# Kernel tuning notes

Measured on AMD Instinct MI355X. Metric: run time of the kernel, lower is better.

Reference implementation:

```python
import jax, jax.numpy as jnp
import numpy as np

D_MODEL = 1024
NUM_HEADS = 16
D_K = D_MODEL // NUM_HEADS


def setup_inputs() -> dict:
    key = jax.random.key(0)
    ks = jax.random.split(key, 8)
    B, S, D = 4, 2048, D_MODEL
    scale = 1.0 / np.sqrt(D)
    return {
        "query": jax.random.normal(ks[0], (B, S, D), dtype=jnp.float32),
        "key": jax.random.normal(ks[1], (B, S, D), dtype=jnp.float32),
        "value": jax.random.normal(ks[2], (B, S, D), dtype=jnp.float32),
        "Wq": jax.random.normal(ks[3], (D, D), dtype=jnp.float32) * scale,
        "bq": jnp.zeros((D,), dtype=jnp.float32),
        "Wk": jax.random.normal(ks[4], (D, D), dtype=jnp.float32) * scale,
        "bk": jnp.zeros((D,), dtype=jnp.float32),
        "Wv": jax.random.normal(ks[5], (D, D), dtype=jnp.float32) * scale,
        "bv": jnp.zeros((D,), dtype=jnp.float32),
        "Wo": jax.random.normal(ks[6], (D, D), dtype=jnp.float32) * scale,
        "bo": jnp.zeros((D,), dtype=jnp.float32),
    }


def reference(query, key, value, Wq, bq, Wk, bk, Wv, bv, Wo, bo):
    B, S, D = query.shape
    H, dk = NUM_HEADS, D_K

    def proj(x, W, b):
        # nn.Linear: x @ W.T + b, then split heads -> [B, H, S, dk]
        y = jnp.einsum("bsd,ed->bse", x, W) + b
        return y.reshape(B, -1, H, dk).transpose(0, 2, 1, 3)

    Q = proj(query, Wq, bq)
    K = proj(key, Wk, bk)
    V = proj(value, Wv, bv)

    scores = jnp.einsum("bhqd,bhkd->bhqk", Q, K) / np.sqrt(dk).astype(jnp.float32)
    attn = jax.nn.softmax(scores, axis=-1)
    out = jnp.einsum("bhqk,bhkd->bhqd", attn, V)  # [B, H, S, dk]
    out = out.transpose(0, 2, 1, 3).reshape(B, -1, D)
    return jnp.einsum("bsd,ed->bse", out, Wo) + bo
```

## Files before the change

### kernel.cpp

```cpp
#include <hip/hip_runtime.h>
#include <hip/hip_bf16.h>

typedef unsigned short u16;
typedef __attribute__((ext_vector_type(8))) short bf16x8;
typedef __attribute__((ext_vector_type(4))) short bf16x4;
typedef __attribute__((ext_vector_type(4))) float f32x4;

#define LOG2E_OVER8 0.18033688011112043f

__device__ __forceinline__ float ex2(float x) {
#if __has_builtin(__builtin_amdgcn_exp2f)
    return __builtin_amdgcn_exp2f(x);
#else
    float r;
    asm volatile("v_exp_f32 %0, %1" : "=v"(r) : "v"(x));
    return r;
#endif
}

__device__ __forceinline__ u16 f2bf(float f) {
    unsigned u = __float_as_uint(f);
    u += 0x7FFFu + ((u >> 16) & 1u);
    return (u16)(u >> 16);
}

__device__ __forceinline__ unsigned pk_rtz(float lo, float hi) {
    return __builtin_amdgcn_perm(__float_as_uint(hi), __float_as_uint(lo), 0x07060302u);
}
__device__ __forceinline__ bf16x8 pack8(float a0, float a1, float a2, float a3,
                                        float a4, float a5, float a6, float a7) {
    unsigned p[4];
    p[0] = pk_rtz(a0, a1);
    p[1] = pk_rtz(a2, a3);
    p[2] = pk_rtz(a4, a5);
    p[3] = pk_rtz(a6, a7);
    bf16x8 r;
    __builtin_memcpy(&r, p, 16);
    return r;
}

__device__ __forceinline__ unsigned pk_rhu(float lo, float hi) {
    unsigned a = __float_as_uint(lo) + 0x8000u;
    unsigned b = __float_as_uint(hi) + 0x8000u;
    return __builtin_amdgcn_perm(b, a, 0x07060302u);
}

__device__ __forceinline__ f32x4 mfma32(bf16x8 a, bf16x8 b, f32x4 c) {
    return __builtin_amdgcn_mfma_f32_16x16x32_bf16(a, b, c, 0, 0, 0);
}

__device__ __forceinline__ void gload16(const void* g, void* l) {
    __builtin_amdgcn_global_load_lds((const __attribute__((address_space(1))) unsigned int*)g,
                                     (__attribute__((address_space(3))) unsigned int*)l,
                                     16, 0, 0);
}

__global__ __launch_bounds__(256) void cvt_w4(const float* __restrict__ a, const float* __restrict__ b,
                                              const float* __restrict__ c, const float* __restrict__ d,
                                              u16* __restrict__ out) {
    const float* src = (blockIdx.y == 0) ? a : (blockIdx.y == 1) ? b : (blockIdx.y == 2) ? c : d;
    size_t i = ((size_t)blockIdx.x * 256 + threadIdx.x) * 4;
    float4 v = *(const float4*)(src + i);
    bf16x4 o;
    o[0] = (short)f2bf(v.x); o[1] = (short)f2bf(v.y);
    o[2] = (short)f2bf(v.z); o[3] = (short)f2bf(v.w);
    *(bf16x4*)(out + (size_t)blockIdx.y * (1024ull * 1024) + i) = o;
}

struct GemmAcc { f32x4 a[4][4]; };

__device__ __forceinline__ void gemm_core(const u16* __restrict__ A, const u16* __restrict__ Bt,
                                          u16* As, u16* Bs, int bm, int bn, GemmAcc& acc) {
    constexpr int K = 1024;
    const int tid = threadIdx.x;
    const int lane = tid & 63;
    const int lr = lane & 15, lg = lane >> 4;
    const int l7 = lr & 7;

    for (int i = 0; i < 4; i++)
        for (int j = 0; j < 4; j++) acc.a[i][j] = (f32x4){0.f, 0.f, 0.f, 0.f};

    const int row0 = tid >> 3, u0 = tid & 7;
    const int su = (u0 ^ (row0 & 7)) * 8;
    size_t a_off[4], b_off[4];
#pragma unroll
    for (int i = 0; i < 4; i++) {
        a_off[i] = (size_t)(bm + i * 32 + row0) * K + su;
        b_off[i] = (size_t)(bn + i * 32 + row0) * K + su;
    }
    const int c0 = tid * 8;
    const int wid = tid >> 6, wr = wid >> 1, wc = wid & 1;

    for (int kt = 0; kt < K; kt += 64) {
#pragma unroll
        for (int i = 0; i < 4; i++) gload16(A + a_off[i] + kt, &As[i * 2048 + c0]);
#pragma unroll
        for (int i = 0; i < 4; i++) gload16(Bt + b_off[i] + kt, &Bs[i * 2048 + c0]);
        __syncthreads();
#pragma unroll
        for (int kh = 0; kh < 2; kh++) {
            const int fu = ((kh * 4 + lg) ^ l7) * 8;
            bf16x8 aF[4], bF[4];
#pragma unroll
            for (int mi = 0; mi < 4; mi++) aF[mi] = *(const bf16x8*)&As[(wr * 64 + mi * 16 + lr) * 64 + fu];
#pragma unroll
            for (int ni = 0; ni < 4; ni++) bF[ni] = *(const bf16x8*)&Bs[(wc * 64 + ni * 16 + lr) * 64 + fu];
#pragma unroll
            for (int mi = 0; mi < 4; mi++)
#pragma unroll
                for (int ni = 0; ni < 4; ni++) acc.a[mi][ni] = mfma32(aF[mi], bF[ni], acc.a[mi][ni]);
        }
        __syncthreads();
    }
}

template<int MODE>
__global__ __launch_bounds__(256, 2) void gemm_f32a(const float* __restrict__ A, const u16* __restrict__ Bt,
                                                    const float* __restrict__ bias, u16* __restrict__ Cout,
                                                    float scale) {
    __shared__ u16 As[128 * 64];
    __shared__ u16 Bs[128 * 64];
    const int tid = threadIdx.x;
    const int bid = blockIdx.x;
    const int m_ = bid & 63, n_ = bid >> 6;
    const int bm = m_ * 128, bn = n_ * 128;
    const int lane = tid & 63;
    const int lr = lane & 15, lg = lane >> 4;
    const int l7 = lr & 7;

    f32x4 acc[4][4];
    for (int i = 0; i < 4; i++)
        for (int j = 0; j < 4; j++) acc[i][j] = (f32x4){0.f, 0.f, 0.f, 0.f};

    const int row0 = tid >> 3, u0 = tid & 7;
    const int su = (u0 ^ (row0 & 7)) * 8;
    size_t b_off[4];
#pragma unroll
    for (int i = 0; i < 4; i++) b_off[i] = (size_t)(bn + i * 32 + row0) * 1024 + su;
    const int c0 = tid * 8;

    const int ar = tid >> 4;
    const size_t a_base = (size_t)(bm + ar) * 1024 + (tid & 15) * 4;
    const int wds = ar * 64 + ((((tid & 15) >> 1) ^ (ar & 7)) << 3) + (tid & 1) * 4;

    float4 fA[2][8];
#pragma unroll
    for (int j = 0; j < 8; ++j) fA[0][j] = *(const float4*)(A + a_base + (size_t)j * 16384);

    const int wid = tid >> 6, wr = wid >> 1, wc = wid & 1;

#pragma unroll 2
    for (int t = 0; t < 16; ++t) {
        const int cur = t & 1;
        const int kt = t * 64;
#pragma unroll
        for (int i = 0; i < 4; i++) gload16(Bt + b_off[i] + kt, &Bs[i * 2048 + c0]);
        const int ktn = ((t + 1) & 15) * 64;
#pragma unroll
        for (int j = 0; j < 8; ++j) fA[cur ^ 1][j] = *(const float4*)(A + a_base + ktn + (size_t)j * 16384);
#pragma unroll
        for (int j = 0; j < 8; ++j) {
            const float4 v = fA[cur][j];
            unsigned p2[2];
            p2[0] = pk_rhu(v.x, v.y);
            p2[1] = pk_rhu(v.z, v.w);
            __builtin_memcpy(&As[wds + j * 1024], p2, 8);
        }
        __syncthreads();
#pragma unroll
        for (int kh = 0; kh < 2; kh++) {
            const int fu = ((kh * 4 + lg) ^ l7) * 8;
            bf16x8 aF[4], bF[4];
#pragma unroll
            for (int mi = 0; mi < 4; mi++) aF[mi] = *(const bf16x8*)&As[(wr * 64 + mi * 16 + lr) * 64 + fu];
#pragma unroll
            for (int ni = 0; ni < 4; ni++) bF[ni] = *(const bf16x8*)&Bs[(wc * 64 + ni * 16 + lr) * 64 + fu];
#pragma unroll
            for (int mi = 0; mi < 4; mi++)
#pragma unroll
                for (int ni = 0; ni < 4; ni++) acc[mi][ni] = mfma32(aF[mi], bF[ni], acc[mi][ni]);
        }
        __syncthreads();
    }

#pragma unroll
    for (int ni = 0; ni < 4; ni++) {
        const int n = bn + wc * 64 + ni * 16 + lr;
        const float bv = bias[n];
#pragma unroll
        for (int mi = 0; mi < 4; mi++) {
            const int mbase = bm + wr * 64 + mi * 16 + lg * 4;
#pragma unroll
            for (int r = 0; r < 4; r++) {
                const int m = mbase + r;
                const float v = acc[mi][ni][r] + bv;
                if (MODE == 1) {
                    Cout[(size_t)m * 1024 + n] = f2bf(v * scale);
                } else {
                    const int bq_ = m >> 11, kk = m & 2047, kb = kk >> 6, k64 = kk & 63;
                    const int hh = n >> 6, dd = n & 63;
                    const int ks = k64 >> 4, g = (k64 >> 2) & 3, rr = k64 & 3;
                    const int unit = ((ks >> 1) << 2) | g;
                    const int jj = ((ks & 1) << 2) | rr;
                    Cout[((size_t)((bq_ * 16 + hh) * 32 + kb)) * 4096 +
                         dd * 64 + ((unit ^ (dd & 7)) << 3) + jj] = f2bf(v);
                }
            }
        }
    }
}

__global__ __launch_bounds__(256) void gemm_out(const u16* __restrict__ A, const u16* __restrict__ Bt,
                                                const float* __restrict__ bias, float* __restrict__ Cout) {
    __shared__ u16 As[128 * 64];
    __shared__ u16 Bs[128 * 64];
    const int bid = blockIdx.x;
    const int m_ = bid & 63, n_ = bid >> 6;
    const int bm = m_ * 128, bn = n_ * 128;
    GemmAcc acc;
    gemm_core(A, Bt, As, Bs, bm, bn, acc);

    const int lane = threadIdx.x & 63, wid = threadIdx.x >> 6;
    const int wr = wid >> 1, wc = wid & 1;
    const int lr = lane & 15, lg = lane >> 4;
#pragma unroll
    for (int ni = 0; ni < 4; ni++) {
        const int n = bn + wc * 64 + ni * 16 + lr;
        const float bv = bias[n];
#pragma unroll
        for (int mi = 0; mi < 4; mi++) {
            const int mbase = bm + wr * 64 + mi * 16 + lg * 4;
#pragma unroll
            for (int r = 0; r < 4; r++)
                Cout[(size_t)(mbase + r) * 1024 + n] = acc.a[mi][ni][r] + bv;
        }
    }
}

__global__ __launch_bounds__(256, 2) void attn_fwd(const u16* __restrict__ Qp, const u16* __restrict__ Kp,
                                                   const u16* __restrict__ VTb, u16* __restrict__ AO) {
    __shared__ u16 kt[2][4096];
    __shared__ u16 vt[2][4096];
    const int tid = threadIdx.x;
    const int lane = tid & 63, wave = tid >> 6;
    const int lr = lane & 15, lg = lane >> 4;
    const int l7 = lr & 7;
    const int bh = blockIdx.x & 63, b = bh >> 4, h = bh & 15;
    const int q0 = (blockIdx.x >> 6) * 256 + wave * 64;

    const u16* qbase = Qp + (size_t)(b * 2048 + q0) * 1024 + h * 64;
    bf16x8 qf[4][2];
#pragma unroll
    for (int qt = 0; qt < 4; qt++)
#pragma unroll
        for (int hf = 0; hf < 2; hf++)
            qf[qt][hf] = *(const bf16x8*)(qbase + (size_t)(qt * 16 + lr) * 1024 + hf * 32 + lg * 8);

    const int srow = tid >> 3;
    const int scol = (((tid & 7) ^ (srow & 7)) * 8);
    const u16* kg = Kp + (size_t)(b * 2048 + srow) * 1024 + h * 64 + scol;
    const u16* vg = VTb + (size_t)(b * 16 + h) * 32 * 4096 + tid * 8;
    const int ldst = tid * 8;

#define STAGE(buf, kb_)                                                       \
    do {                                                                      \
        gload16(kg + (size_t)(kb_) * 64 * 1024,        &kt[buf][ldst]);       \
        gload16(kg + (size_t)((kb_) * 64 + 32) * 1024, &kt[buf][2048 + ldst]);\
        gload16(vg + (size_t)(kb_) * 4096,             &vt[buf][ldst]);       \
        gload16(vg + (size_t)(kb_) * 4096 + 2048,      &vt[buf][2048 + ldst]);\
    } while (0)

    f32x4 lsacc[4];
    f32x4 ot[4][4];
#pragma unroll
    for (int qt = 0; qt < 4; qt++) {
        lsacc[qt] = (f32x4){0.f, 0.f, 0.f, 0.f};
#pragma unroll
        for (int dt = 0; dt < 4; dt++) ot[qt][dt] = (f32x4){0.f, 0.f, 0.f, 0.f};
    }

    bf16x8 ones8;
#pragma unroll
    for (int i = 0; i < 8; i++) ones8[i] = (short)0x3F80;

    STAGE(0, 0);
    __syncthreads();
    int cur = 0;

    const f32x4 zero = (f32x4){0.f, 0.f, 0.f, 0.f};
    const int ku0 = (lg ^ l7) * 8;
    const int ku1 = ((4 + lg) ^ l7) * 8;

#pragma unroll 2
    for (int it = 0; it < 32; ++it) {
        if (it < 31) STAGE(cur ^ 1, it + 1);

        const u16* kl = &kt[cur][0];
        const u16* vl = &vt[cur][0];

        f32x4 s[4][4];
        __builtin_amdgcn_s_setprio(1);
#pragma unroll
        for (int ks = 0; ks < 4; ++ks) {
            const int rbase = (ks * 16 + lr) * 64;
            bf16x8 kf0 = *(const bf16x8*)&kl[rbase + ku0];
            bf16x8 kf1 = *(const bf16x8*)&kl[rbase + ku1];
#pragma unroll
            for (int qt = 0; qt < 4; ++qt) {
                s[qt][ks] = mfma32(kf0, qf[qt][0], zero);
                s[qt][ks] = mfma32(kf1, qf[qt][1], s[qt][ks]);
            }
        }
        __builtin_amdgcn_s_setprio(0);

        bf16x8 pf[4][2];
#pragma unroll
        for (int qt = 0; qt < 4; ++qt) {
#pragma unroll
            for (int kh = 0; kh < 2; ++kh) {
                const f32x4 sa = s[qt][2 * kh], sb = s[qt][2 * kh + 1];
                pf[qt][kh] = pack8(ex2(sa[0]), ex2(sa[1]), ex2(sa[2]), ex2(sa[3]),
                                   ex2(sb[0]), ex2(sb[1]), ex2(sb[2]), ex2(sb[3]));
                lsacc[qt] = mfma32(ones8, pf[qt][kh], lsacc[qt]);
            }
        }

        __builtin_amdgcn_s_setprio(1);
#pragma unroll
        for (int dt = 0; dt < 4; ++dt) {
            const int vrow = (dt * 16 + lr) * 64;
            bf16x8 vf0 = *(const bf16x8*)&vl[vrow + ku0];
            bf16x8 vf1 = *(const bf16x8*)&vl[vrow + ku1];
#pragma unroll
            for (int qt = 0; qt < 4; ++qt) {
                ot[qt][dt] = mfma32(vf0, pf[qt][0], ot[qt][dt]);
                ot[qt][dt] = mfma32(vf1, pf[qt][1], ot[qt][dt]);
            }
        }
        __builtin_amdgcn_s_setprio(0);

        __syncthreads();
        cur ^= 1;
    }

    float inv[4];
#pragma unroll
    for (int qt = 0; qt < 4; qt++) inv[qt] = 1.0f / lsacc[qt][0];
    u16* t_ = &kt[0][0] + wave * 2048;
#pragma unroll
    for (int pass = 0; pass < 2; ++pass) {
        __syncthreads();
#pragma unroll
        for (int qh = 0; qh < 2; ++qh) {
            const int qt = pass * 2 + qh;
#pragma unroll
            for (int dt = 0; dt < 4; ++dt)
#pragma unroll
                for (int r = 0; r < 4; ++r)
                    t_[(qh * 16 + lr) * 64 + dt * 16 + lg * 4 + r] = f2bf(ot[qt][dt][r] * inv[qt]);
        }
        __syncthreads();
        const int qq = lane >> 1, dseg = (lane & 1) * 32;
        u16* dst = AO + (size_t)(b * 2048 + q0 + pass * 32 + qq) * 1024 + h * 64 + dseg;
        bf16x8 o_[4];
#pragma unroll
        for (int j = 0; j < 4; ++j) o_[j] = *(const bf16x8*)&t_[qq * 64 + dseg + j * 8];
#pragma unroll
        for (int j = 0; j < 4; ++j) *(bf16x8*)(dst + j * 8) = o_[j];
    }
#undef STAGE
}

extern "C" void kernel_launch(void* const* d_in, const int* in_sizes, int n_in,
                              void* d_out, int out_size, void* d_ws, size_t ws_size,
                              hipStream_t stream) {
    const float* q_in = (const float*)d_in[0];
    const float* k_in = (const float*)d_in[1];
    const float* v_in = (const float*)d_in[2];
    const float* Wq = (const float*)d_in[3];
    const float* bq = (const float*)d_in[4];
    const float* Wk = (const float*)d_in[5];
    const float* bk = (const float*)d_in[6];
    const float* Wv = (const float*)d_in[7];
    const float* bv = (const float*)d_in[8];
    const float* Wo = (const float*)d_in[9];
    const float* bo = (const float*)d_in[10];

    const size_t MD = (size_t)8192 * 1024;
    const size_t DD = (size_t)1024 * 1024;
    u16* ws = (u16*)d_ws;
    u16* Wqb = ws;
    u16* Wkb = Wqb + DD;
    u16* Wvb = Wkb + DD;
    u16* Wob = Wvb + DD;
    u16* Qp = Wqb + 4 * DD;
    u16* Kp = Qp + MD;
    u16* VTb = Kp + MD;
    u16* AO = VTb + MD;

    cvt_w4<<<dim3(1024, 4), 256, 0, stream>>>(Wq, Wk, Wv, Wo, Wqb);

    gemm_f32a<1><<<512, 256, 0, stream>>>(q_in, Wqb, bq, Qp, LOG2E_OVER8);
    gemm_f32a<1><<<512, 256, 0, stream>>>(k_in, Wkb, bk, Kp, 1.0f);
    gemm_f32a<2><<<512, 256, 0, stream>>>(v_in, Wvb, bv, VTb, 1.0f);

    attn_fwd<<<512, 256, 0, stream>>>(Qp, Kp, VTb, AO);

    gemm_out<<<512, 256, 0, stream>>>(AO, Wob, bo, (float*)d_out);
}
```

Measured before the change: 183.0 us.

## Give each wave private K/V LDS buffers and drop block-wide barriers in attention

```diff
diff --git a/kernel.cpp b/kernel.cpp
--- a/kernel.cpp
+++ b/kernel.cpp
@@ -197,13 +197,11 @@
                 if (MODE == 1) {
                     Cout[(size_t)m * 1024 + n] = f2bf(v * scale);
                 } else {
-                    const int bq_ = m >> 11, kk = m & 2047, kb = kk >> 6, k64 = kk & 63;
+                    const int bq_ = m >> 11, kk = m & 2047, kb = kk >> 5, k32 = kk & 31;
                     const int hh = n >> 6, dd = n & 63;
-                    const int ks = k64 >> 4, g = (k64 >> 2) & 3, rr = k64 & 3;
-                    const int unit = ((ks >> 1) << 2) | g;
-                    const int jj = ((ks & 1) << 2) | rr;
-                    Cout[((size_t)((bq_ * 16 + hh) * 32 + kb)) * 4096 +
-                         dd * 64 + ((unit ^ (dd & 7)) << 3) + jj] = f2bf(v);
+                    const int ks = k32 >> 4, g = (k32 >> 2) & 3, rr = k32 & 3;
+                    Cout[((size_t)((bq_ * 16 + hh) * 64 + kb)) * 2048 +
+                         dd * 32 + g * 8 + (ks << 2) + rr] = f2bf(v);
                 }
             }
         }
@@ -239,14 +237,19 @@
 
 __global__ __launch_bounds__(256, 2) void attn_fwd(const u16* __restrict__ Qp, const u16* __restrict__ Kp,
                                                    const u16* __restrict__ VTb, u16* __restrict__ AO) {
-    __shared__ u16 kt[2][4096];
-    __shared__ u16 vt[2][4096];
+    __shared__ u16 lds[4][8192];
     const int tid = threadIdx.x;
     const int lane = tid & 63, wave = tid >> 6;
     const int lr = lane & 15, lg = lane >> 4;
     const int l7 = lr & 7;
-    const int bh = blockIdx.x & 63, b = bh >> 4, h = bh & 15;
-    const int q0 = (blockIdx.x >> 6) * 256 + wave * 64;
+    const int bid = blockIdx.x;
+    const int bh = bid & 63, b = bh >> 4, h = bh & 15;
+    const int q0 = (wave * 8 + (bid >> 6)) * 64;
+
+    u16* kt0 = &lds[wave][0];
+    u16* kt1 = &lds[wave][2048];
+    u16* vt0 = &lds[wave][4096];
+    u16* vt1 = &lds[wave][6144];
 
     const u16* qbase = Qp + (size_t)(b * 2048 + q0) * 1024 + h * 64;
     bf16x8 qf[4][2];
@@ -256,18 +259,22 @@
         for (int hf = 0; hf < 2; hf++)
             qf[qt][hf] = *(const bf16x8*)(qbase + (size_t)(qt * 16 + lr) * 1024 + hf * 32 + lg * 8);
 
-    const int srow = tid >> 3;
-    const int scol = (((tid & 7) ^ (srow & 7)) * 8);
+    const int srow = lane >> 3;
+    const int scol = ((lane & 7) ^ (srow & 7)) * 8;
     const u16* kg = Kp + (size_t)(b * 2048 + srow) * 1024 + h * 64 + scol;
-    const u16* vg = VTb + (size_t)(b * 16 + h) * 32 * 4096 + tid * 8;
-    const int ldst = tid * 8;
-
-#define STAGE(buf, kb_)                                                       \
-    do {                                                                      \
-        gload16(kg + (size_t)(kb_) * 64 * 1024,        &kt[buf][ldst]);       \
-        gload16(kg + (size_t)((kb_) * 64 + 32) * 1024, &kt[buf][2048 + ldst]);\
-        gload16(vg + (size_t)(kb_) * 4096,             &vt[buf][ldst]);       \
-        gload16(vg + (size_t)(kb_) * 4096 + 2048,      &vt[buf][2048 + ldst]);\
+    const u16* vg = VTb + (size_t)(b * 16 + h) * (64 * 2048) + lane * 8;
+    const int kdst = lane * 8;
+
+#define STAGE(kd, vd, t_)                                                        \
+    do {                                                                         \
+        gload16(kg + (size_t)((t_) * 32 +  0) * 1024, (kd) + kdst);              \
+        gload16(kg + (size_t)((t_) * 32 +  8) * 1024, (kd) + 512 + kdst);        \
+        gload16(kg + (size_t)((t_) * 32 + 16) * 1024, (kd) + 1024 + kdst);       \
+        gload16(kg + (size_t)((t_) * 32 + 24) * 1024, (kd) + 1536 + kdst);       \
+        gload16(vg + (size_t)(t_) * 2048,        (vd));                          \
+        gload16(vg + (size_t)(t_) * 2048 + 512,  (vd) + 512);                    \
+        gload16(vg + (size_t)(t_) * 2048 + 1024, (vd) + 1024);                   \
+        gload16(vg + (size_t)(t_) * 2048 + 1536, (vd) + 1536);                   \
     } while (0)
 
     f32x4 lsacc[4];
@@ -282,26 +289,33 @@
     bf16x8 ones8;
 #pragma unroll
     for (int i = 0; i < 8; i++) ones8[i] = (short)0x3F80;
-
-    STAGE(0, 0);
-    __syncthreads();
-    int cur = 0;
 
     const f32x4 zero = (f32x4){0.f, 0.f, 0.f, 0.f};
     const int ku0 = (lg ^ l7) * 8;
     const int ku1 = ((4 + lg) ^ l7) * 8;
+    const int vofs = lg * 8;
+
+    STAGE(kt0, vt0, 0);
 
 #pragma unroll 2
-    for (int it = 0; it < 32; ++it) {
-        if (it < 31) STAGE(cur ^ 1, it + 1);
-
-        const u16* kl = &kt[cur][0];
-        const u16* vl = &vt[cur][0];
-
-        f32x4 s[4][4];
+    for (int t = 0; t < 64; ++t) {
+        const int cur = t & 1;
+        const u16* kl = cur ? kt1 : kt0;
+        const u16* vl = cur ? vt1 : vt0;
+        u16* kn = cur ? kt0 : kt1;
+        u16* vn = cur ? vt0 : vt1;
+
+        if (t < 63) {
+            STAGE(kn, vn, t + 1);
+            asm volatile("s_waitcnt vmcnt(8)" ::: "memory");
+        } else {
+            asm volatile("s_waitcnt vmcnt(0)" ::: "memory");
+        }
+
+        f32x4 s[4][2];
         __builtin_amdgcn_s_setprio(1);
 #pragma unroll
-        for (int ks = 0; ks < 4; ++ks) {
+        for (int ks = 0; ks < 2; ++ks) {
             const int rbase = (ks * 16 + lr) * 64;
             bf16x8 kf0 = *(const bf16x8*)&kl[rbase + ku0];
             bf16x8 kf1 = *(const bf16x8*)&kl[rbase + ku1];
@@ -313,43 +327,32 @@
         }
         __builtin_amdgcn_s_setprio(0);
 
-        bf16x8 pf[4][2];
+        bf16x8 pf[4];
 #pragma unroll
         for (int qt = 0; qt < 4; ++qt) {
-#pragma unroll
-            for (int kh = 0; kh < 2; ++kh) {
-                const f32x4 sa = s[qt][2 * kh], sb = s[qt][2 * kh + 1];
-                pf[qt][kh] = pack8(ex2(sa[0]), ex2(sa[1]), ex2(sa[2]), ex2(sa[3]),
-                                   ex2(sb[0]), ex2(sb[1]), ex2(sb[2]), ex2(sb[3]));
-                lsacc[qt] = mfma32(ones8, pf[qt][kh], lsacc[qt]);
-            }
+            const f32x4 sa = s[qt][0], sb = s[qt][1];
+            pf[qt] = pack8(ex2(sa[0]), ex2(sa[1]), ex2(sa[2]), ex2(sa[3]),
+                           ex2(sb[0]), ex2(sb[1]), ex2(sb[2]), ex2(sb[3]));
+            lsacc[qt] = mfma32(ones8, pf[qt], lsacc[qt]);
         }
 
         __builtin_amdgcn_s_setprio(1);
 #pragma unroll
         for (int dt = 0; dt < 4; ++dt) {
-            const int vrow = (dt * 16 + lr) * 64;
-            bf16x8 vf0 = *(const bf16x8*)&vl[vrow + ku0];
-            bf16x8 vf1 = *(const bf16x8*)&vl[vrow + ku1];
-#pragma unroll
-            for (int qt = 0; qt < 4; ++qt) {
-                ot[qt][dt] = mfma32(vf0, pf[qt][0], ot[qt][dt]);
-                ot[qt][dt] = mfma32(vf1, pf[qt][1], ot[qt][dt]);
-            }
+            bf16x8 vf = *(const bf16x8*)&vl[(dt * 16 + lr) * 32 + vofs];
+#pragma unroll
+            for (int qt = 0; qt < 4; ++qt)
+                ot[qt][dt] = mfma32(vf, pf[qt], ot[qt][dt]);
         }
         __builtin_amdgcn_s_setprio(0);
-
-        __syncthreads();
-        cur ^= 1;
     }
 
     float inv[4];
 #pragma unroll
     for (int qt = 0; qt < 4; qt++) inv[qt] = 1.0f / lsacc[qt][0];
-    u16* t_ = &kt[0][0] + wave * 2048;
+    u16* t_ = kt0;
 #pragma unroll
     for (int pass = 0; pass < 2; ++pass) {
-        __syncthreads();
 #pragma unroll
         for (int qh = 0; qh < 2; ++qh) {
             const int qt = pass * 2 + qh;
@@ -359,7 +362,6 @@
                 for (int r = 0; r < 4; ++r)
                     t_[(qh * 16 + lr) * 64 + dt * 16 + lg * 4 + r] = f2bf(ot[qt][dt][r] * inv[qt]);
         }
-        __syncthreads();
         const int qq = lane >> 1, dseg = (lane & 1) * 32;
         u16* dst = AO + (size_t)(b * 2048 + q0 + pass * 32 + qq) * 1024 + h * 64 + dseg;
         bf16x8 o_[4];
```

New measurement: 187.4 us. 1.02x slower.
